# Kernel optimization log

Measured on AMD Instinct MI355X. Metric: run time of the kernel, lower is better.

## Reference

```python
import jax, jax.numpy as jnp
import numpy as np

D = 256; DFFN = 1024; H = 8; NLVL = 4; NPNT = 4; HD = D // H
BS = 4; NQ = 100; NPTS = 25
SPATIAL = [(128, 128), (64, 64), (32, 32), (16, 16)]
LEN_IN = sum(h * w for h, w in SPATIAL)


def _ln(x, g, b, eps=1e-5):
    m = x.mean(-1, keepdims=True)
    v = ((x - m) ** 2).mean(-1, keepdims=True)
    return (x - m) * jax.lax.rsqrt(v + eps) * g + b


def _mha(q, k, v, w_in, b_in, w_out, b_out):
    # torch nn.MultiheadAttention math, batch-first layout [B,S,D]
    B, Sq, _ = q.shape; Sk = k.shape[1]
    wq, wk, wv = jnp.split(w_in, 3, 0); bq, bk, bv = jnp.split(b_in, 3)
    qh = (q @ wq.T + bq).reshape(B, Sq, H, HD).transpose(0, 2, 1, 3)
    kh = (k @ wk.T + bk).reshape(B, Sk, H, HD).transpose(0, 2, 1, 3)
    vh = (v @ wv.T + bv).reshape(B, Sk, H, HD).transpose(0, 2, 1, 3)
    a = jax.nn.softmax(jnp.einsum('bhqd,bhkd->bhqk', qh, kh) * (1.0 / float(np.sqrt(HD))), -1)
    o = jnp.einsum('bhqk,bhkd->bhqd', a, vh).transpose(0, 2, 1, 3).reshape(B, Sq, D)
    return o @ w_out.T + b_out


def _msdeform(query, ref, src, off_w, off_b, aw_w, aw_b, val_w, val_b, out_w, out_b):
    # MSDeformAttn: per-query multi-level bilinear sampling + weighted aggregation
    bs, Lq, _ = query.shape
    value = (src @ val_w.T + val_b).reshape(bs, LEN_IN, H, HD)
    off = (query @ off_w.T + off_b).reshape(bs, Lq, H, NLVL, NPNT, 2)
    aw = jax.nn.softmax((query @ aw_w.T + aw_b).reshape(bs, Lq, H, NLVL * NPNT), -1)
    aw = aw.reshape(bs, Lq, H, NLVL, NPNT)
    norm = jnp.array([[w, h] for h, w in SPATIAL], jnp.float32)  # (W,H) per level
    loc = ref[:, :, None, :, None, :] + off / norm[None, None, None, :, None, :]
    out = jnp.zeros((bs, H, Lq, HD), query.dtype)
    start = 0
    for l, (hh, ww) in enumerate(SPATIAL):
        v_l = value[:, start:start + hh * ww].transpose(0, 2, 1, 3)  # [bs,H,hw,HD]
        start += hh * ww
        # grid_sample align_corners=False pixel coords: loc*size - 0.5
        x = (loc[:, :, :, l, :, 0] * ww - 0.5).transpose(0, 2, 1, 3).reshape(bs, H, Lq * NPNT)
        y = (loc[:, :, :, l, :, 1] * hh - 0.5).transpose(0, 2, 1, 3).reshape(bs, H, Lq * NPNT)
        x0 = jnp.floor(x); y0 = jnp.floor(y); wx = x - x0; wy = y - y0
        x0i = x0.astype(jnp.int32); y0i = y0.astype(jnp.int32); x1i = x0i + 1; y1i = y0i + 1
        def g(xi, yi):
            valid = ((xi >= 0) & (xi < ww) & (yi >= 0) & (yi < hh)).astype(query.dtype)
            idx = jnp.clip(yi, 0, hh - 1) * ww + jnp.clip(xi, 0, ww - 1)
            return jnp.take_along_axis(v_l, idx[..., None], axis=2) * valid[..., None]
        s = (g(x0i, y0i) * ((1 - wx) * (1 - wy))[..., None]
             + g(x1i, y0i) * (wx * (1 - wy))[..., None]
             + g(x0i, y1i) * ((1 - wx) * wy)[..., None]
             + g(x1i, y1i) * (wx * wy)[..., None])
        s = s.reshape(bs, H, Lq, NPNT, HD)
        out = out + (s * aw[:, :, :, l].transpose(0, 2, 1, 3)[..., None]).sum(3)
    return out.transpose(0, 2, 1, 3).reshape(bs, Lq, D) @ out_w.T + out_b


def _fwd(tgt, query_pos, reference_points, src,
         w_in_intra, b_in_intra, w_out_intra, b_out_intra, g_norm_intra, b_norm_intra,
         w_in_inter, b_in_inter, w_out_inter, b_out_inter, g_norm_inter, b_norm_inter,
         off_w, off_b, aw_w, aw_b, val_w, val_b, co_w, co_b, g_norm_cross, b_norm_cross,
         lin1_w, lin1_b, lin2_w, lin2_b, g_norm3, b_norm3):
    bs, nq, npts, d = tgt.shape
    # intra-instance self-attention (over control points)
    q = (tgt + query_pos).reshape(bs * nq, npts, d)
    t2 = _mha(q, q, tgt.reshape(bs * nq, npts, d), w_in_intra, b_in_intra, w_out_intra, b_out_intra)
    tgt = _ln(tgt + t2.reshape(bs, nq, npts, d), g_norm_intra, b_norm_intra)
    # inter-instance self-attention (over queries), no pos embed per source code
    ti = tgt.transpose(0, 2, 1, 3).reshape(bs * npts, nq, d)
    t2 = _mha(ti, ti, ti, w_in_inter, b_in_inter, w_out_inter, b_out_inter)
    ti = _ln(ti + t2, g_norm_inter, b_norm_inter).reshape(bs, npts, nq, d).transpose(0, 2, 1, 3)
    # deformable cross-attention
    ref = jnp.broadcast_to(reference_points[:, :, None], (bs, nq, npts, NLVL, 2)).reshape(bs, nq * npts, NLVL, 2)
    qc = (ti + query_pos).reshape(bs, nq * npts, d)
    t2 = _msdeform(qc, ref, src, off_w, off_b, aw_w, aw_b, val_w, val_b, co_w, co_b).reshape(bs, nq, npts, d)
    tgt = _ln(ti + t2, g_norm_cross, b_norm_cross)
    # FFN
    ff = jax.nn.relu(tgt @ lin1_w.T + lin1_b) @ lin2_w.T + lin2_b
    return _ln(tgt + ff, g_norm3, b_norm3)


def setup_inputs() -> dict:
    key = jax.random.key(0)
    ki = iter(jax.random.split(key, 40))
    def rn(shape, sc=0.02):
        return jax.random.normal(next(ki), shape, jnp.float32) * sc
    inp = dict(
        tgt=jax.random.normal(next(ki), (BS, NQ, NPTS, D), jnp.float32),
        query_pos=jax.random.normal(next(ki), (BS, NQ, NPTS, D), jnp.float32),
        reference_points=jax.random.uniform(next(ki), (BS, NQ, NLVL, 2), jnp.float32),
        src=jax.random.normal(next(ki), (BS, LEN_IN, D), jnp.float32),
        w_in_intra=rn((3 * D, D)), b_in_intra=jnp.zeros((3 * D,), jnp.float32),
        w_out_intra=rn((D, D)), b_out_intra=jnp.zeros((D,), jnp.float32),
        g_norm_intra=jnp.ones((D,), jnp.float32), b_norm_intra=jnp.zeros((D,), jnp.float32),
        w_in_inter=rn((3 * D, D)), b_in_inter=jnp.zeros((3 * D,), jnp.float32),
        w_out_inter=rn((D, D)), b_out_inter=jnp.zeros((D,), jnp.float32),
        g_norm_inter=jnp.ones((D,), jnp.float32), b_norm_inter=jnp.zeros((D,), jnp.float32),
        off_w=rn((H * NLVL * NPNT * 2, D), 0.001), off_b=rn((H * NLVL * NPNT * 2,), 0.5),
        aw_w=rn((H * NLVL * NPNT, D)), aw_b=jnp.zeros((H * NLVL * NPNT,), jnp.float32),
        val_w=rn((D, D)), val_b=jnp.zeros((D,), jnp.float32),
        co_w=rn((D, D)), co_b=jnp.zeros((D,), jnp.float32),
        g_norm_cross=jnp.ones((D,), jnp.float32), b_norm_cross=jnp.zeros((D,), jnp.float32),
        lin1_w=rn((DFFN, D)), lin1_b=jnp.zeros((DFFN,), jnp.float32),
        lin2_w=rn((D, DFFN)), lin2_b=jnp.zeros((D,), jnp.float32),
        g_norm3=jnp.ones((D,), jnp.float32), b_norm3=jnp.zeros((D,), jnp.float32),
        src_spatial_shapes=jnp.array(SPATIAL, jnp.int32),
        level_start_index=jnp.array(np.cumsum([0] + [h * w for h, w in SPATIAL[:-1]]), jnp.int32),
    )
    return inp


def reference(tgt, query_pos, reference_points, src,
              w_in_intra, b_in_intra, w_out_intra, b_out_intra, g_norm_intra, b_norm_intra,
              w_in_inter, b_in_inter, w_out_inter, b_out_inter, g_norm_inter, b_norm_inter,
              off_w, off_b, aw_w, aw_b, val_w, val_b, co_w, co_b, g_norm_cross, b_norm_cross,
              lin1_w, lin1_b, lin2_w, lin2_b, g_norm3, b_norm3,
              src_spatial_shapes, level_start_index):
    # spatial shapes / level starts are compile-time constants (SPATIAL); args kept for signature parity
    return _fwd(tgt, query_pos, reference_points, src,
                w_in_intra, b_in_intra, w_out_intra, b_out_intra, g_norm_intra, b_norm_intra,
                w_in_inter, b_in_inter, w_out_inter, b_out_inter, g_norm_inter, b_norm_inter,
                off_w, off_b, aw_w, aw_b, val_w, val_b, co_w, co_b, g_norm_cross, b_norm_cross,
                lin1_w, lin1_b, lin2_w, lin2_b, g_norm3, b_norm3)
```

## Files before the change

### kernel.cpp

```cpp
#include <hip/hip_runtime.h>
#include <math.h>

#define DMODEL 256
#define HEADS  8
#define HDIM   32
#define BS     4
#define NQ     100
#define NPTS   25
#define LQ     2500
#define M10K   10000
#define LEN_IN 21760
#define MVAL   87040

typedef float f32x4 __attribute__((ext_vector_type(4)));
typedef short s16x8 __attribute__((ext_vector_type(8)));
typedef unsigned short u16;

static __device__ __forceinline__ short f2bf(float f) {
    unsigned u = __builtin_bit_cast(unsigned, f);
    u = (u + 0x7fffu + ((u >> 16) & 1u)) >> 16;
    return (short)u;
}
static __device__ __forceinline__ unsigned pack2(float lo, float hi) {
    return (unsigned)(u16)f2bf(lo) | ((unsigned)(u16)f2bf(hi) << 16);
}
static __device__ __forceinline__ float bf_lo(unsigned u) {
    return __builtin_bit_cast(float, u << 16);
}
static __device__ __forceinline__ float bf_hi(unsigned u) {
    return __builtin_bit_cast(float, u & 0xffff0000u);
}

#define LDSK   40
#define LDSK64 72

__global__ __launch_bounds__(256) void convert_weights_kernel(
    const float* __restrict__ s0, const float* __restrict__ s1,
    const float* __restrict__ s2, const float* __restrict__ s3,
    const float* __restrict__ s4, const float* __restrict__ s5,
    const float* __restrict__ s6, const float* __restrict__ s7,
    const float* __restrict__ s8, const float* __restrict__ s9,
    u16* __restrict__ dst)
{
    int t8 = (blockIdx.x * 256 + threadIdx.x) * 8;
    if (t8 >= 1277952) return;
    const float* s; int base;
    if      (t8 <  196608) { s = s0; base = 0;       }
    else if (t8 <  262144) { s = s1; base = 196608;  }
    else if (t8 <  458752) { s = s2; base = 262144;  }
    else if (t8 <  524288) { s = s3; base = 458752;  }
    else if (t8 <  589824) { s = s4; base = 524288;  }
    else if (t8 <  622592) { s = s5; base = 589824;  }
    else if (t8 <  688128) { s = s6; base = 622592;  }
    else if (t8 <  753664) { s = s7; base = 688128;  }
    else if (t8 < 1015808) { s = s8; base = 753664;  }
    else                   { s = s9; base = 1015808; }
    const float* p = s + (t8 - base);
    float4 a = *(const float4*)p;
    float4 b = *(const float4*)(p + 4);
    s16x8 v;
    v[0]=f2bf(a.x); v[1]=f2bf(a.y); v[2]=f2bf(a.z); v[3]=f2bf(a.w);
    v[4]=f2bf(b.x); v[5]=f2bf(b.y); v[6]=f2bf(b.z); v[7]=f2bf(b.w);
    *(s16x8*)(dst + t8) = v;
}

__global__ __launch_bounds__(256) void add_convert_kernel(
    const float* __restrict__ a, const float* __restrict__ b,
    u16* __restrict__ xb, u16* __restrict__ ab, int n8)
{
    int i = blockIdx.x * 256 + threadIdx.x;
    if (i >= n8) return;
    size_t o = (size_t)i * 8;
    float4 a0 = *(const float4*)(a + o);
    float4 a1 = *(const float4*)(a + o + 4);
    if (ab) {
        s16x8 v;
        v[0]=f2bf(a0.x); v[1]=f2bf(a0.y); v[2]=f2bf(a0.z); v[3]=f2bf(a0.w);
        v[4]=f2bf(a1.x); v[5]=f2bf(a1.y); v[6]=f2bf(a1.z); v[7]=f2bf(a1.w);
        *(s16x8*)(ab + o) = v;
    }
    if (b) {
        float4 b0 = *(const float4*)(b + o);
        float4 b1 = *(const float4*)(b + o + 4);
        a0.x += b0.x; a0.y += b0.y; a0.z += b0.z; a0.w += b0.w;
        a1.x += b1.x; a1.y += b1.y; a1.z += b1.z; a1.w += b1.w;
    }
    s16x8 v;
    v[0]=f2bf(a0.x); v[1]=f2bf(a0.y); v[2]=f2bf(a0.z); v[3]=f2bf(a0.w);
    v[4]=f2bf(a1.x); v[5]=f2bf(a1.y); v[6]=f2bf(a1.z); v[7]=f2bf(a1.w);
    *(s16x8*)(xb + o) = v;
}

__global__ __launch_bounds__(256) void gemm_mfma_kernel(
    const u16* __restrict__ A, int lda,
    const u16* __restrict__ W, int K,
    const float* __restrict__ bias,
    void* __restrict__ Cv, int ldc,
    int M, int relu, int out_bf16)
{
    __shared__ short As[64 * LDSK64];
    __shared__ short Ws[64 * LDSK64];

    const int tid = threadIdx.x;
    const int m0 = blockIdx.y * 64, n0 = blockIdx.x * 64;
    const int srow = tid >> 2;
    const int sk = (tid & 3) * 16;
    const int wave = tid >> 6;
    const int wm = wave & 1, wn = wave >> 1;
    const int lane = tid & 63;
    const int lrow = lane & 15;
    const int kq = lane >> 4;

    const int gm = m0 + srow;
    const u16* aptr = A + (size_t)gm * lda + sk;
    const u16* wptr = W + (size_t)(n0 + srow) * K + sk;

    f32x4 acc[2][2];
#pragma unroll
    for (int i = 0; i < 2; ++i)
#pragma unroll
        for (int j = 0; j < 2; ++j) acc[i][j] = (f32x4)(0.f);

    s16x8 a0 = (s16x8)0, a1 = (s16x8)0, w0, w1;
    if (gm < M) { a0 = *(const s16x8*)aptr; a1 = *(const s16x8*)(aptr + 8); }
    w0 = *(const s16x8*)wptr; w1 = *(const s16x8*)(wptr + 8);

    for (int k0 = 0; k0 < K; k0 += 64) {
        *(s16x8*)&As[srow * LDSK64 + sk]     = a0;
        *(s16x8*)&As[srow * LDSK64 + sk + 8] = a1;
        *(s16x8*)&Ws[srow * LDSK64 + sk]     = w0;
        *(s16x8*)&Ws[srow * LDSK64 + sk + 8] = w1;
        __syncthreads();
        if (k0 + 64 < K) {
            if (gm < M) {
                a0 = *(const s16x8*)(aptr + k0 + 64);
                a1 = *(const s16x8*)(aptr + k0 + 72);
            }
            w0 = *(const s16x8*)(wptr + k0 + 64);
            w1 = *(const s16x8*)(wptr + k0 + 72);
        }

#pragma unroll
        for (int s = 0; s < 2; ++s) {
            s16x8 af[2], bfv[2];
#pragma unroll
            for (int i = 0; i < 2; ++i)
                af[i] = *(const s16x8*)&As[(wm * 32 + i * 16 + lrow) * LDSK64 + s * 32 + kq * 8];
#pragma unroll
            for (int j = 0; j < 2; ++j)
                bfv[j] = *(const s16x8*)&Ws[(wn * 32 + j * 16 + lrow) * LDSK64 + s * 32 + kq * 8];
#pragma unroll
            for (int i = 0; i < 2; ++i)
#pragma unroll
                for (int j = 0; j < 2; ++j)
                    acc[i][j] = __builtin_amdgcn_mfma_f32_16x16x32_bf16(af[i], bfv[j], acc[i][j], 0, 0, 0);
        }
        __syncthreads();
    }

#pragma unroll
    for (int i = 0; i < 2; ++i)
#pragma unroll
        for (int j = 0; j < 2; ++j) {
            int col = n0 + wn * 32 + j * 16 + lrow;
            float bv = bias[col];
#pragma unroll
            for (int reg = 0; reg < 4; ++reg) {
                int gmo = m0 + wm * 32 + i * 16 + kq * 4 + reg;
                if (gmo < M) {
                    float v = acc[i][j][reg] + bv;
                    if (relu) v = fmaxf(v, 0.f);
                    if (out_bf16)
                        ((u16*)Cv)[(size_t)gmo * ldc + col] = (u16)f2bf(v);
                    else
                        ((float*)Cv)[(size_t)gmo * ldc + col] = v;
                }
            }
        }
}

__global__ __launch_bounds__(256) void gemm_mfma128_kernel(
    const u16* __restrict__ A, int lda,
    const u16* __restrict__ W, int K,
    const float* __restrict__ bias,
    void* __restrict__ Cv, int ldc,
    int M, int relu, int out_bf16)
{
    __shared__ short As[128 * LDSK];
    __shared__ short Ws[128 * LDSK];

    const int tid = threadIdx.x;
    const int m0 = blockIdx.y * 128, n0 = blockIdx.x * 128;

    const int srow = tid >> 1;
    const int sk = (tid & 1) * 16;

    const int wave = tid >> 6;
    const int wm = wave & 1, wn = wave >> 1;
    const int lane = tid & 63;
    const int lrow = lane & 15;
    const int kq = lane >> 4;

    const int gm = m0 + srow;
    const u16* aptr = A + (size_t)gm * lda + sk;
    const u16* wptr = W + (size_t)(n0 + srow) * K + sk;

    f32x4 acc[4][4];
#pragma unroll
    for (int i = 0; i < 4; ++i)
#pragma unroll
        for (int j = 0; j < 4; ++j) acc[i][j] = (f32x4)(0.f);

    s16x8 a0 = (s16x8)0, a1 = (s16x8)0, w0, w1;
    if (gm < M) { a0 = *(const s16x8*)aptr; a1 = *(const s16x8*)(aptr + 8); }
    w0 = *(const s16x8*)wptr; w1 = *(const s16x8*)(wptr + 8);

    for (int k0 = 0; k0 < K; k0 += 32) {
        *(s16x8*)&As[srow * LDSK + sk]     = a0;
        *(s16x8*)&As[srow * LDSK + sk + 8] = a1;
        *(s16x8*)&Ws[srow * LDSK + sk]     = w0;
        *(s16x8*)&Ws[srow * LDSK + sk + 8] = w1;
        __syncthreads();
        if (k0 + 32 < K) {
            if (gm < M) {
                a0 = *(const s16x8*)(aptr + k0 + 32);
                a1 = *(const s16x8*)(aptr + k0 + 40);
            }
            w0 = *(const s16x8*)(wptr + k0 + 32);
            w1 = *(const s16x8*)(wptr + k0 + 40);
        }

        s16x8 af[4], bfv[4];
#pragma unroll
        for (int i = 0; i < 4; ++i)
            af[i] = *(const s16x8*)&As[(wm * 64 + i * 16 + lrow) * LDSK + kq * 8];
#pragma unroll
        for (int j = 0; j < 4; ++j)
            bfv[j] = *(const s16x8*)&Ws[(wn * 64 + j * 16 + lrow) * LDSK + kq * 8];
#pragma unroll
        for (int i = 0; i < 4; ++i)
#pragma unroll
            for (int j = 0; j < 4; ++j)
                acc[i][j] = __builtin_amdgcn_mfma_f32_16x16x32_bf16(af[i], bfv[j], acc[i][j], 0, 0, 0);
        __syncthreads();
    }

#pragma unroll
    for (int i = 0; i < 4; ++i)
#pragma unroll
        for (int j = 0; j < 4; ++j) {
            int col = n0 + wn * 64 + j * 16 + lrow;
            float bv = bias[col];
#pragma unroll
            for (int reg = 0; reg < 4; ++reg) {
                int gmo = m0 + wm * 64 + i * 16 + kq * 4 + reg;
                if (gmo < M) {
                    float v = acc[i][j][reg] + bv;
                    if (relu) v = fmaxf(v, 0.f);
                    if (out_bf16)
                        ((u16*)Cv)[(size_t)gmo * ldc + col] = (u16)f2bf(v);
                    else
                        ((float*)Cv)[(size_t)gmo * ldc + col] = v;
                }
            }
        }
}

__global__ __launch_bounds__(256) void gemm_value64_kernel(
    const float* __restrict__ A,
    const u16* __restrict__ W,
    const float* __restrict__ bias,
    u16* __restrict__ C)
{
    __shared__ short As[64 * LDSK];
    __shared__ short Ws[128 * LDSK];

    const int tid = threadIdx.x;
    const int n0 = blockIdx.x * 128;
    const int m0 = blockIdx.y * 64;

    const int arow = tid >> 2;
    const int ak = (tid & 3) * 8;
    const int wrow = tid >> 1;
    const int wk = (tid & 1) * 16;

    const float* aptr = A + (size_t)(m0 + arow) * 256 + ak;
    const u16* wptr = W + (size_t)(n0 + wrow) * 256 + wk;

    const int wave = tid >> 6;
    const int wm = wave & 1, wn = wave >> 1;
    const int lane = tid & 63;
    const int lrow = lane & 15, kq = lane >> 4;

    f32x4 acc[2][4];
#pragma unroll
    for (int i = 0; i < 2; ++i)
#pragma unroll
        for (int j = 0; j < 4; ++j) acc[i][j] = (f32x4)(0.f);

    float4 pa0 = *(const float4*)aptr;
    float4 pa1 = *(const float4*)(aptr + 4);
    s16x8 w0 = *(const s16x8*)wptr;
    s16x8 w1 = *(const s16x8*)(wptr + 8);

    for (int k0 = 0; k0 < 256; k0 += 32) {
        s16x8 av;
        av[0]=f2bf(pa0.x); av[1]=f2bf(pa0.y); av[2]=f2bf(pa0.z); av[3]=f2bf(pa0.w);
        av[4]=f2bf(pa1.x); av[5]=f2bf(pa1.y); av[6]=f2bf(pa1.z); av[7]=f2bf(pa1.w);
        *(s16x8*)&As[arow * LDSK + ak]     = av;
        *(s16x8*)&Ws[wrow * LDSK + wk]     = w0;
        *(s16x8*)&Ws[wrow * LDSK + wk + 8] = w1;
        __syncthreads();
        if (k0 + 32 < 256) {
            pa0 = *(const float4*)(aptr + k0 + 32);
            pa1 = *(const float4*)(aptr + k0 + 36);
            w0 = *(const s16x8*)(wptr + k0 + 32);
            w1 = *(const s16x8*)(wptr + k0 + 40);
        }

        s16x8 af[2], bfv[4];
#pragma unroll
        for (int i = 0; i < 2; ++i)
            af[i] = *(const s16x8*)&As[(wm * 32 + i * 16 + lrow) * LDSK + kq * 8];
#pragma unroll
        for (int j = 0; j < 4; ++j)
            bfv[j] = *(const s16x8*)&Ws[(wn * 64 + j * 16 + lrow) * LDSK + kq * 8];
#pragma unroll
        for (int i = 0; i < 2; ++i)
#pragma unroll
            for (int j = 0; j < 4; ++j)
                acc[i][j] = __builtin_amdgcn_mfma_f32_16x16x32_bf16(af[i], bfv[j], acc[i][j], 0, 0, 0);
        __syncthreads();
    }

#pragma unroll
    for (int i = 0; i < 2; ++i)
#pragma unroll
        for (int j = 0; j < 4; ++j) {
            int col = n0 + wn * 64 + j * 16 + lrow;
            float bv = bias[col];
#pragma unroll
            for (int reg = 0; reg < 4; ++reg) {
                int gmo = m0 + wm * 32 + i * 16 + kq * 4 + reg;
                C[(size_t)gmo * 256 + col] = (u16)f2bf(acc[i][j][reg] + bv);
            }
        }
}

__global__ __launch_bounds__(256) void inter_attn_mfma_kernel(
    const u16* __restrict__ qkv, u16* __restrict__ out, float scale)
{
    __shared__ __align__(16) u16 Qs[112 * 40];
    __shared__ __align__(16) u16 Ks[112 * 40];
    __shared__ __align__(16) u16 Vt[32 * 136];
    __shared__ __align__(16) u16 Ps[112 * 136];

    const int b = blockIdx.x, h = blockIdx.y;
    const u16* base = qkv + (size_t)b * 100 * 768;
    const int tid = threadIdx.x;
    const int wave = tid >> 6, lane = tid & 63;
    const int lr = lane & 15, quad = lane >> 4;

    for (int i = tid; i < 12 * 20; i += 256) {
        int row = 100 + i / 20, c = (i % 20) * 2;
        *(unsigned*)&Qs[row * 40 + c] = 0;
        *(unsigned*)&Ks[row * 40 + c] = 0;
    }
    for (int i = tid; i < 2176; i += 256) ((unsigned*)Vt)[i] = 0;
    for (int i = tid; i < 7616; i += 256) ((unsigned*)Ps)[i] = 0;
    __syncthreads();

    for (int idx = tid; idx < 2400; idx += 256) {
        int row = idx / 24, s = idx % 24;
        const u16* p = (s < 8)  ? base + row * 768 + h * 32 + s * 4
                     : (s < 16) ? base + row * 768 + 256 + h * 32 + (s - 8) * 4
                                : base + row * 768 + 512 + h * 32 + (s - 16) * 4;
        if (s < 8) {
// ... 116 lines not shown
                float4 kf = kr[c4];
                dot = fmaf(q[c4*4+0], kf.x, dot);
                dot = fmaf(q[c4*4+1], kf.y, dot);
                dot = fmaf(q[c4*4+2], kf.z, dot);
                dot = fmaf(q[c4*4+3], kf.w, dot);
            }
            dot *= scale;
            float mn = fmaxf(m, dot);
            float alpha = __expf(m - mn);
            float p = __expf(dot - mn);
            l = l * alpha + p;
            const float4* vr = &KV[j][64 + h * 8];
#pragma unroll
            for (int c4 = 0; c4 < 8; ++c4) {
                float4 vf = vr[c4];
                acc[c4*4+0] = acc[c4*4+0] * alpha + p * vf.x;
                acc[c4*4+1] = acc[c4*4+1] * alpha + p * vf.y;
                acc[c4*4+2] = acc[c4*4+2] * alpha + p * vf.z;
                acc[c4*4+3] = acc[c4*4+3] * alpha + p * vf.w;
            }
            m = mn;
        }
        float inv = 1.f / l;
        unsigned* op = (unsigned*)(out + ((size_t)b * 25 + r) * 256 + h * 32);
#pragma unroll
        for (int c = 0; c < 16; ++c)
            op[c] = pack2(acc[2*c] * inv, acc[2*c+1] * inv);
    }
}

__global__ __launch_bounds__(64) void add_ln_kernel(
    const float* __restrict__ a, const float* __restrict__ b,
    const float* __restrict__ g, const float* __restrict__ beta,
    float* __restrict__ out, u16* __restrict__ out_bf, int transpose_mode)
{
    const int r = blockIdx.x;
    const int lane = threadIdx.x;
    const float* ar = a + (size_t)r * 256;
    const float* br = b + (size_t)r * 256;
    float x[4];
    float s = 0.f;
#pragma unroll
    for (int i = 0; i < 4; ++i) {
        x[i] = ar[lane + 64 * i] + br[lane + 64 * i];
        s += x[i];
    }
#pragma unroll
    for (int off = 32; off >= 1; off >>= 1) s += __shfl_xor(s, off);
    float mean = s * (1.f / 256.f);
    float vs = 0.f;
#pragma unroll
    for (int i = 0; i < 4; ++i) { float d = x[i] - mean; vs += d * d; }
#pragma unroll
    for (int off = 32; off >= 1; off >>= 1) vs += __shfl_xor(vs, off);
    float rstd = rsqrtf(vs * (1.f / 256.f) + 1e-5f);

    size_t ro = r;
    if (transpose_mode == 1) {
        int q = r % 100; int bp = r / 100; int p = bp % 25; int bb = bp / 25;
        ro = ((size_t)bb * 100 + q) * 25 + p;
    } else if (transpose_mode == 2) {
        int p = r % 25; int t = r / 25; int q = t % 100; int bb = t / 100;
        ro = ((size_t)bb * 25 + p) * 100 + q;
    }
    float* orow = out + ro * 256;
    u16* brow = out_bf ? out_bf + ro * 256 : (u16*)0;
#pragma unroll
    for (int i = 0; i < 4; ++i) {
        int c = lane + 64 * i;
        float v = (x[i] - mean) * rstd * g[c] + beta[c];
        orow[c] = v;
        if (brow) brow[c] = (u16)f2bf(v);
    }
}

__global__ __launch_bounds__(256, 4) void msdeform_sample_kernel(
    const u16* __restrict__ value,
    const float* __restrict__ off,
    const float* __restrict__ awl,
    const float* __restrict__ refp,
    u16* __restrict__ sampled)
{
    const int unit = blockIdx.x * 8 + (threadIdx.x >> 5);
    const int t = threadIdx.x & 31;
    const int h = t >> 2, c8 = t & 3;
    const int b = unit / LQ, lq = unit - b * LQ;
    const int q = lq / NPTS;

    const float* awp = awl + (size_t)unit * 128 + h * 16;
    float w[16];
    float mx = -1e30f;
#pragma unroll
    for (int k = 0; k < 16; ++k) { w[k] = awp[k]; mx = fmaxf(mx, w[k]); }
    float sum = 0.f;
#pragma unroll
    for (int k = 0; k < 16; ++k) { w[k] = __expf(w[k] - mx); sum += w[k]; }
    const float inv = 1.f / sum;

    const float* offp = off + (size_t)unit * 256 + h * 32;
    const float* rp = refp + ((size_t)b * 100 + q) * 8;
    const u16* vbase = value + (size_t)b * LEN_IN * 256 + h * 32 + c8 * 8;

    float acc[8];
#pragma unroll
    for (int k = 0; k < 8; ++k) acc[k] = 0.f;
// ... 85 lines not shown
    const float* co_b       = (const float*)d_in[23];
    const float* g_ln_cross = (const float*)d_in[24];
    const float* b_ln_cross = (const float*)d_in[25];
    const float* lin1_w     = (const float*)d_in[26];
    const float* lin1_b     = (const float*)d_in[27];
    const float* lin2_w     = (const float*)d_in[28];
    const float* lin2_b     = (const float*)d_in[29];
    const float* g_ln3      = (const float*)d_in[30];
    const float* b_ln3      = (const float*)d_in[31];

    float* ws    = (float*)d_ws;
    float* qkv   = ws;
    float* tmp   = ws + 7680000;
    u16*   attnb = (u16*)(ws + 10240000);
    float* tgt1  = ws + 11520000;
    float* ti    = ws + 14080000;
    u16*   tib   = (u16*)(ws + 16640000);
    float* tA    = ws + 17920000;
    u16*   qcb   = (u16*)(ws + 20480000);
    u16*   x1b   = (u16*)(ws + 21760000);
    u16*   tgtb  = (u16*)(ws + 23040000);
    float* awl   = ws + 24320000;
    u16*   valueb= (u16*)(ws + 25600000);
    u16*   wb    = (u16*)(ws + 36741120);
    float* out   = (float*)d_out;

    u16* qkvb = (u16*)qkv;

    u16* wb_in_intra  = wb;
    u16* wb_out_intra = wb + 196608;
    u16* wb_in_inter  = wb + 262144;
    u16* wb_out_inter = wb + 458752;
    u16* wb_off       = wb + 524288;
    u16* wb_aw        = wb + 589824;
    u16* wb_val       = wb + 622592;
    u16* wb_co        = wb + 688128;
    u16* wb_lin1      = wb + 753664;
    u16* wb_lin2      = wb + 1015808;

    const float scale = 0.17677669529663687f;
    const int MB64  = (M10K + 63) / 64;
    const int MB128 = (M10K + 127) / 128;

    convert_weights_kernel<<<624, 256, 0, stream>>>(
        w_in_intra, w_out_intra, w_in_inter, w_out_inter, off_w,
        aw_w, val_w, co_w, lin1_w, lin2_w, wb);
    add_convert_kernel<<<1250, 256, 0, stream>>>(tgt, query_pos, x1b, tgtb, 320000);

    gemm_mfma128_kernel<<<dim3(4, MB128), 256, 0, stream>>>(x1b, 256, wb_in_intra, 256,
                                                            b_in_intra, qkv, 768, M10K, 0, 0);
    gemm_mfma_kernel<<<dim3(4, MB64), 256, 0, stream>>>(tgtb, 256, wb_in_intra + 512 * 256, 256,
                                                        b_in_intra + 512, qkv + 512, 768, M10K, 0, 0);
    intra_attn_kernel<<<400, 256, 0, stream>>>(qkv, attnb, scale);
    gemm_mfma_kernel<<<dim3(4, MB64), 256, 0, stream>>>(attnb, 256, wb_out_intra, 256,
                                                        b_out_intra, tmp, 256, M10K, 0, 0);
    add_ln_kernel<<<M10K, 64, 0, stream>>>(tgt, tmp, g_ln_intra, b_ln_intra, ti, tib, 2);

    gemm_mfma128_kernel<<<dim3(6, MB128), 256, 0, stream>>>(tib, 256, wb_in_inter, 256,
                                                            b_in_inter, qkvb, 768, M10K, 0, 1);
    inter_attn_mfma_kernel<<<dim3(100, 8), 256, 0, stream>>>(qkvb, attnb, scale);
    gemm_mfma_kernel<<<dim3(4, MB64), 256, 0, stream>>>(attnb, 256, wb_out_inter, 256,
                                                        b_out_inter, tmp, 256, M10K, 0, 0);
    add_ln_kernel<<<M10K, 64, 0, stream>>>(ti, tmp, g_ln_inter, b_ln_inter, tA, (u16*)0, 1);

    add_convert_kernel<<<1250, 256, 0, stream>>>(tA, query_pos, qcb, (u16*)0, 320000);
    gemm_value64_kernel<<<dim3(2, 1360), 256, 0, stream>>>(src, wb_val, val_b, valueb);
    gemm_mfma_kernel<<<dim3(4, MB64), 256, 0, stream>>>(qcb, 256, wb_off, 256,
                                                        off_b, tgt1, 256, M10K, 0, 0);
    gemm_mfma_kernel<<<dim3(2, MB64), 256, 0, stream>>>(qcb, 256, wb_aw, 256,
                                                        aw_b, awl, 128, M10K, 0, 0);
    msdeform_sample_kernel<<<1250, 256, 0, stream>>>(valueb, tgt1, awl, refp, attnb);
    gemm_mfma_kernel<<<dim3(4, MB64), 256, 0, stream>>>(attnb, 256, wb_co, 256,
                                                        co_b, tmp, 256, M10K, 0, 0);
    add_ln_kernel<<<M10K, 64, 0, stream>>>(tA, tmp, g_ln_cross, b_ln_cross, ti, tib, 0);

    gemm_mfma128_kernel<<<dim3(8, MB128), 256, 0, stream>>>(tib, 256, wb_lin1, 256,
                                                            lin1_b, valueb, 1024, M10K, 1, 1);
    gemm_mfma_kernel<<<dim3(4, MB64), 256, 0, stream>>>(valueb, 1024, wb_lin2, 1024,
                                                        lin2_b, tmp, 256, M10K, 0, 0);
    add_ln_kernel<<<M10K, 64, 0, stream>>>(ti, tmp, g_ln3, b_ln3, out, (u16*)0, 0);
}
```

Before: 479.2 us.

## Merge independent launches into fat kernels and fuse query_pos add into LayerNorm

Weight conversion and the tgt/query_pos conversion now run as one launch, selected by block index. The value projection and the intra-attention QKV GEMMs are merged into one multi-role launch, so the large value GEMM overlaps with the QKV work. The offset and attention-weight GEMMs share one launch through a column split, and the query_pos add plus bf16 conversion moves into the inter LayerNorm epilogue, removing one elementwise kernel. This cuts launch count and idle tails, at the cost of mixed-role blocks with different shared-memory and register needs, which may lower occupancy.

```diff
diff --git a/kernel.cpp b/kernel.cpp
--- a/kernel.cpp
+++ b/kernel.cpp
@@ -34,250 +34,68 @@
 #define LDSK   40
 #define LDSK64 72
 
-__global__ __launch_bounds__(256) void convert_weights_kernel(
+__global__ __launch_bounds__(256) void fat_stage0_kernel(
     const float* __restrict__ s0, const float* __restrict__ s1,
     const float* __restrict__ s2, const float* __restrict__ s3,
     const float* __restrict__ s4, const float* __restrict__ s5,
     const float* __restrict__ s6, const float* __restrict__ s7,
     const float* __restrict__ s8, const float* __restrict__ s9,
-    u16* __restrict__ dst)
-{
-    int t8 = (blockIdx.x * 256 + threadIdx.x) * 8;
-    if (t8 >= 1277952) return;
-    const float* s; int base;
-    if      (t8 <  196608) { s = s0; base = 0;       }
-    else if (t8 <  262144) { s = s1; base = 196608;  }
-    else if (t8 <  458752) { s = s2; base = 262144;  }
-    else if (t8 <  524288) { s = s3; base = 458752;  }
-    else if (t8 <  589824) { s = s4; base = 524288;  }
-    else if (t8 <  622592) { s = s5; base = 589824;  }
-    else if (t8 <  688128) { s = s6; base = 622592;  }
-    else if (t8 <  753664) { s = s7; base = 688128;  }
-    else if (t8 < 1015808) { s = s8; base = 753664;  }
-    else                   { s = s9; base = 1015808; }
-    const float* p = s + (t8 - base);
-    float4 a = *(const float4*)p;
-    float4 b = *(const float4*)(p + 4);
-    s16x8 v;
-    v[0]=f2bf(a.x); v[1]=f2bf(a.y); v[2]=f2bf(a.z); v[3]=f2bf(a.w);
-    v[4]=f2bf(b.x); v[5]=f2bf(b.y); v[6]=f2bf(b.z); v[7]=f2bf(b.w);
-    *(s16x8*)(dst + t8) = v;
-}
-
-__global__ __launch_bounds__(256) void add_convert_kernel(
+    u16* __restrict__ dst,
     const float* __restrict__ a, const float* __restrict__ b,
-    u16* __restrict__ xb, u16* __restrict__ ab, int n8)
-{
-    int i = blockIdx.x * 256 + threadIdx.x;
-    if (i >= n8) return;
-    size_t o = (size_t)i * 8;
-    float4 a0 = *(const float4*)(a + o);
-    float4 a1 = *(const float4*)(a + o + 4);
-    if (ab) {
+    u16* __restrict__ xb, u16* __restrict__ ab)
+{
+    if (blockIdx.x < 624) {
+        int t8 = (blockIdx.x * 256 + threadIdx.x) * 8;
+        if (t8 >= 1277952) return;
+        const float* s; int base;
+        if      (t8 <  196608) { s = s0; base = 0;       }
+        else if (t8 <  262144) { s = s1; base = 196608;  }
+        else if (t8 <  458752) { s = s2; base = 262144;  }
+        else if (t8 <  524288) { s = s3; base = 458752;  }
+        else if (t8 <  589824) { s = s4; base = 524288;  }
+        else if (t8 <  622592) { s = s5; base = 589824;  }
+        else if (t8 <  688128) { s = s6; base = 622592;  }
+        else if (t8 <  753664) { s = s7; base = 688128;  }
+        else if (t8 < 1015808) { s = s8; base = 753664;  }
+        else                   { s = s9; base = 1015808; }
+        const float* p = s + (t8 - base);
+        float4 fa = *(const float4*)p;
+        float4 fb = *(const float4*)(p + 4);
+        s16x8 v;
+        v[0]=f2bf(fa.x); v[1]=f2bf(fa.y); v[2]=f2bf(fa.z); v[3]=f2bf(fa.w);
+        v[4]=f2bf(fb.x); v[5]=f2bf(fb.y); v[6]=f2bf(fb.z); v[7]=f2bf(fb.w);
+        *(s16x8*)(dst + t8) = v;
+    } else {
+        int i = (blockIdx.x - 624) * 256 + threadIdx.x;
+        size_t o = (size_t)i * 8;
+        float4 a0 = *(const float4*)(a + o);
+        float4 a1 = *(const float4*)(a + o + 4);
         s16x8 v;
         v[0]=f2bf(a0.x); v[1]=f2bf(a0.y); v[2]=f2bf(a0.z); v[3]=f2bf(a0.w);
         v[4]=f2bf(a1.x); v[5]=f2bf(a1.y); v[6]=f2bf(a1.z); v[7]=f2bf(a1.w);
         *(s16x8*)(ab + o) = v;
-    }
-    if (b) {
         float4 b0 = *(const float4*)(b + o);
         float4 b1 = *(const float4*)(b + o + 4);
         a0.x += b0.x; a0.y += b0.y; a0.z += b0.z; a0.w += b0.w;
         a1.x += b1.x; a1.y += b1.y; a1.z += b1.z; a1.w += b1.w;
-    }
-    s16x8 v;
-    v[0]=f2bf(a0.x); v[1]=f2bf(a0.y); v[2]=f2bf(a0.z); v[3]=f2bf(a0.w);
-    v[4]=f2bf(a1.x); v[5]=f2bf(a1.y); v[6]=f2bf(a1.z); v[7]=f2bf(a1.w);
-    *(s16x8*)(xb + o) = v;
-}
-
-__global__ __launch_bounds__(256) void gemm_mfma_kernel(
-    const u16* __restrict__ A, int lda,
-    const u16* __restrict__ W, int K,
-    const float* __restrict__ bias,
-    void* __restrict__ Cv, int ldc,
-    int M, int relu, int out_bf16)
-{
-    __shared__ short As[64 * LDSK64];
-    __shared__ short Ws[64 * LDSK64];
+        s16x8 w;
+        w[0]=f2bf(a0.x); w[1]=f2bf(a0.y); w[2]=f2bf(a0.z); w[3]=f2bf(a0.w);
+        w[4]=f2bf(a1.x); w[5]=f2bf(a1.y); w[6]=f2bf(a1.z); w[7]=f2bf(a1.w);
+        *(s16x8*)(xb + o) = w;
+    }
+}
+
+
+static __device__ __forceinline__ void body_value64(
+    char* smem_, const float* __restrict__ A, const u16* __restrict__ W,
+    const float* __restrict__ bias, u16* __restrict__ C, int bx, int by)
+{
+    short* As = (short*)smem_;
+    short* Ws = (short*)(smem_ + 5120);
 
     const int tid = threadIdx.x;
-    const int m0 = blockIdx.y * 64, n0 = blockIdx.x * 64;
-    const int srow = tid >> 2;
-    const int sk = (tid & 3) * 16;
-    const int wave = tid >> 6;
-    const int wm = wave & 1, wn = wave >> 1;
-    const int lane = tid & 63;
-    const int lrow = lane & 15;
-    const int kq = lane >> 4;
-
-    const int gm = m0 + srow;
-    const u16* aptr = A + (size_t)gm * lda + sk;
-    const u16* wptr = W + (size_t)(n0 + srow) * K + sk;
-
-    f32x4 acc[2][2];
-#pragma unroll
-    for (int i = 0; i < 2; ++i)
-#pragma unroll
-        for (int j = 0; j < 2; ++j) acc[i][j] = (f32x4)(0.f);
-
-    s16x8 a0 = (s16x8)0, a1 = (s16x8)0, w0, w1;
-    if (gm < M) { a0 = *(const s16x8*)aptr; a1 = *(const s16x8*)(aptr + 8); }
-    w0 = *(const s16x8*)wptr; w1 = *(const s16x8*)(wptr + 8);
-
-    for (int k0 = 0; k0 < K; k0 += 64) {
-        *(s16x8*)&As[srow * LDSK64 + sk]     = a0;
-        *(s16x8*)&As[srow * LDSK64 + sk + 8] = a1;
-        *(s16x8*)&Ws[srow * LDSK64 + sk]     = w0;
-        *(s16x8*)&Ws[srow * LDSK64 + sk + 8] = w1;
-        __syncthreads();
-        if (k0 + 64 < K) {
-            if (gm < M) {
-                a0 = *(const s16x8*)(aptr + k0 + 64);
-                a1 = *(const s16x8*)(aptr + k0 + 72);
-            }
-            w0 = *(const s16x8*)(wptr + k0 + 64);
-            w1 = *(const s16x8*)(wptr + k0 + 72);
-        }
-
-#pragma unroll
-        for (int s = 0; s < 2; ++s) {
-            s16x8 af[2], bfv[2];
-#pragma unroll
-            for (int i = 0; i < 2; ++i)
-                af[i] = *(const s16x8*)&As[(wm * 32 + i * 16 + lrow) * LDSK64 + s * 32 + kq * 8];
-#pragma unroll
-            for (int j = 0; j < 2; ++j)
-                bfv[j] = *(const s16x8*)&Ws[(wn * 32 + j * 16 + lrow) * LDSK64 + s * 32 + kq * 8];
-#pragma unroll
-            for (int i = 0; i < 2; ++i)
-#pragma unroll
-                for (int j = 0; j < 2; ++j)
-                    acc[i][j] = __builtin_amdgcn_mfma_f32_16x16x32_bf16(af[i], bfv[j], acc[i][j], 0, 0, 0);
-        }
-        __syncthreads();
-    }
-
-#pragma unroll
-    for (int i = 0; i < 2; ++i)
-#pragma unroll
-        for (int j = 0; j < 2; ++j) {
-            int col = n0 + wn * 32 + j * 16 + lrow;
-            float bv = bias[col];
-#pragma unroll
-            for (int reg = 0; reg < 4; ++reg) {
-                int gmo = m0 + wm * 32 + i * 16 + kq * 4 + reg;
-                if (gmo < M) {
-                    float v = acc[i][j][reg] + bv;
-                    if (relu) v = fmaxf(v, 0.f);
-                    if (out_bf16)
-                        ((u16*)Cv)[(size_t)gmo * ldc + col] = (u16)f2bf(v);
-                    else
-                        ((float*)Cv)[(size_t)gmo * ldc + col] = v;
-                }
-            }
-        }
-}
-
-__global__ __launch_bounds__(256) void gemm_mfma128_kernel(
-    const u16* __restrict__ A, int lda,
-    const u16* __restrict__ W, int K,
-    const float* __restrict__ bias,
-    void* __restrict__ Cv, int ldc,
-    int M, int relu, int out_bf16)
-{
-    __shared__ short As[128 * LDSK];
-    __shared__ short Ws[128 * LDSK];
-
-    const int tid = threadIdx.x;
-    const int m0 = blockIdx.y * 128, n0 = blockIdx.x * 128;
-
-    const int srow = tid >> 1;
-    const int sk = (tid & 1) * 16;
-
-    const int wave = tid >> 6;
-    const int wm = wave & 1, wn = wave >> 1;
-    const int lane = tid & 63;
-    const int lrow = lane & 15;
-    const int kq = lane >> 4;
-
-    const int gm = m0 + srow;
-    const u16* aptr = A + (size_t)gm * lda + sk;
-    const u16* wptr = W + (size_t)(n0 + srow) * K + sk;
-
-    f32x4 acc[4][4];
-#pragma unroll
-    for (int i = 0; i < 4; ++i)
-#pragma unroll
-        for (int j = 0; j < 4; ++j) acc[i][j] = (f32x4)(0.f);
-
-    s16x8 a0 = (s16x8)0, a1 = (s16x8)0, w0, w1;
-    if (gm < M) { a0 = *(const s16x8*)aptr; a1 = *(const s16x8*)(aptr + 8); }
-    w0 = *(const s16x8*)wptr; w1 = *(const s16x8*)(wptr + 8);
-
-    for (int k0 = 0; k0 < K; k0 += 32) {
-        *(s16x8*)&As[srow * LDSK + sk]     = a0;
-        *(s16x8*)&As[srow * LDSK + sk + 8] = a1;
-        *(s16x8*)&Ws[srow * LDSK + sk]     = w0;
-        *(s16x8*)&Ws[srow * LDSK + sk + 8] = w1;
-        __syncthreads();
-        if (k0 + 32 < K) {
-            if (gm < M) {
-                a0 = *(const s16x8*)(aptr + k0 + 32);
-                a1 = *(const s16x8*)(aptr + k0 + 40);
-            }
-            w0 = *(const s16x8*)(wptr + k0 + 32);
-            w1 = *(const s16x8*)(wptr + k0 + 40);
-        }
-
-        s16x8 af[4], bfv[4];
-#pragma unroll
-        for (int i = 0; i < 4; ++i)
-            af[i] = *(const s16x8*)&As[(wm * 64 + i * 16 + lrow) * LDSK + kq * 8];
-#pragma unroll
-        for (int j = 0; j < 4; ++j)
-            bfv[j] = *(const s16x8*)&Ws[(wn * 64 + j * 16 + lrow) * LDSK + kq * 8];
-#pragma unroll
-        for (int i = 0; i < 4; ++i)
-#pragma unroll
-            for (int j = 0; j < 4; ++j)
-                acc[i][j] = __builtin_amdgcn_mfma_f32_16x16x32_bf16(af[i], bfv[j], acc[i][j], 0, 0, 0);
-        __syncthreads();
-    }
-
-#pragma unroll
-    for (int i = 0; i < 4; ++i)
-#pragma unroll
-        for (int j = 0; j < 4; ++j) {
-            int col = n0 + wn * 64 + j * 16 + lrow;
-            float bv = bias[col];
-#pragma unroll
-            for (int reg = 0; reg < 4; ++reg) {
-                int gmo = m0 + wm * 64 + i * 16 + kq * 4 + reg;
-                if (gmo < M) {
-                    float v = acc[i][j][reg] + bv;
-                    if (relu) v = fmaxf(v, 0.f);
-                    if (out_bf16)
-                        ((u16*)Cv)[(size_t)gmo * ldc + col] = (u16)f2bf(v);
-                    else
-                        ((float*)Cv)[(size_t)gmo * ldc + col] = v;
-                }
-            }
-        }
-}
-
-__global__ __launch_bounds__(256) void gemm_value64_kernel(
-    const float* __restrict__ A,
-    const u16* __restrict__ W,
-    const float* __restrict__ bias,
-    u16* __restrict__ C)
-{
-    __shared__ short As[64 * LDSK];
-    __shared__ short Ws[128 * LDSK];
-
-    const int tid = threadIdx.x;
-    const int n0 = blockIdx.x * 128;
-    const int m0 = blockIdx.y * 64;
+    const int n0 = bx * 128;
+    const int m0 = by * 64;
 
     const int arow = tid >> 2;
     const int ak = (tid & 3) * 8;
@@ -343,6 +161,361 @@
             for (int reg = 0; reg < 4; ++reg) {
                 int gmo = m0 + wm * 32 + i * 16 + kq * 4 + reg;
                 C[(size_t)gmo * 256 + col] = (u16)f2bf(acc[i][j][reg] + bv);
+            }
+        }
+}
+
+static __device__ __forceinline__ void body_mfma128(
+    char* smem_, const u16* __restrict__ A, const u16* __restrict__ W,
+    const float* __restrict__ bias, float* __restrict__ Cv, int bx, int by)
+{
+    short* As = (short*)smem_;
+    short* Ws = (short*)(smem_ + 10240);
+
+    const int tid = threadIdx.x;
+    const int m0 = by * 128, n0 = bx * 128;
+    const int srow = tid >> 1;
+    const int sk = (tid & 1) * 16;
+    const int wave = tid >> 6;
+    const int wm = wave & 1, wn = wave >> 1;
+    const int lane = tid & 63;
+    const int lrow = lane & 15, kq = lane >> 4;
+
+    const int gm = m0 + srow;
+    const u16* aptr = A + (size_t)gm * 256 + sk;
+    const u16* wptr = W + (size_t)(n0 + srow) * 256 + sk;
+
+    f32x4 acc[4][4];
+#pragma unroll
+    for (int i = 0; i < 4; ++i)
+#pragma unroll
+        for (int j = 0; j < 4; ++j) acc[i][j] = (f32x4)(0.f);
+
+    s16x8 a0 = (s16x8)0, a1 = (s16x8)0, w0, w1;
+    if (gm < M10K) { a0 = *(const s16x8*)aptr; a1 = *(const s16x8*)(aptr + 8); }
+    w0 = *(const s16x8*)wptr; w1 = *(const s16x8*)(wptr + 8);
+
+    for (int k0 = 0; k0 < 256; k0 += 32) {
+        *(s16x8*)&As[srow * LDSK + sk]     = a0;
+        *(s16x8*)&As[srow * LDSK + sk + 8] = a1;
+        *(s16x8*)&Ws[srow * LDSK + sk]     = w0;
+        *(s16x8*)&Ws[srow * LDSK + sk + 8] = w1;
+        __syncthreads();
+        if (k0 + 32 < 256) {
+            if (gm < M10K) {
+                a0 = *(const s16x8*)(aptr + k0 + 32);
+                a1 = *(const s16x8*)(aptr + k0 + 40);
+            }
+            w0 = *(const s16x8*)(wptr + k0 + 32);
+            w1 = *(const s16x8*)(wptr + k0 + 40);
+        }
+
+        s16x8 af[4], bfv[4];
+#pragma unroll
+        for (int i = 0; i < 4; ++i)
+            af[i] = *(const s16x8*)&As[(wm * 64 + i * 16 + lrow) * LDSK + kq * 8];
+#pragma unroll
+        for (int j = 0; j < 4; ++j)
+            bfv[j] = *(const s16x8*)&Ws[(wn * 64 + j * 16 + lrow) * LDSK + kq * 8];
+#pragma unroll
+        for (int i = 0; i < 4; ++i)
+#pragma unroll
+            for (int j = 0; j < 4; ++j)
+                acc[i][j] = __builtin_amdgcn_mfma_f32_16x16x32_bf16(af[i], bfv[j], acc[i][j], 0, 0, 0);
+        __syncthreads();
+    }
+
+#pragma unroll
+    for (int i = 0; i < 4; ++i)
+#pragma unroll
+        for (int j = 0; j < 4; ++j) {
+            int col = n0 + wn * 64 + j * 16 + lrow;
+            float bv = bias[col];
+#pragma unroll
+            for (int reg = 0; reg < 4; ++reg) {
+                int gmo = m0 + wm * 64 + i * 16 + kq * 4 + reg;
+                if (gmo < M10K)
+                    Cv[(size_t)gmo * 768 + col] = acc[i][j][reg] + bv;
+            }
+        }
+}
+
+static __device__ __forceinline__ void body_mfma64(
+    char* smem_, const u16* __restrict__ A, const u16* __restrict__ W,
+    const float* __restrict__ bias, float* __restrict__ Cv, int bx, int by)
+{
+    short* As = (short*)smem_;
+    short* Ws = (short*)(smem_ + 9216);
+
+    const int tid = threadIdx.x;
+    const int m0 = by * 64, n0 = bx * 64;
+    const int srow = tid >> 2;
+    const int sk = (tid & 3) * 16;
+    const int wave = tid >> 6;
+    const int wm = wave & 1, wn = wave >> 1;
+    const int lane = tid & 63;
+    const int lrow = lane & 15, kq = lane >> 4;
+
+    const int gm = m0 + srow;
+    const u16* aptr = A + (size_t)gm * 256 + sk;
+    const u16* wptr = W + (size_t)(n0 + srow) * 256 + sk;
+
+    f32x4 acc[2][2];
+#pragma unroll
+    for (int i = 0; i < 2; ++i)
+#pragma unroll
+        for (int j = 0; j < 2; ++j) acc[i][j] = (f32x4)(0.f);
+
+    s16x8 a0 = (s16x8)0, a1 = (s16x8)0, w0, w1;
+    if (gm < M10K) { a0 = *(const s16x8*)aptr; a1 = *(const s16x8*)(aptr + 8); }
+    w0 = *(const s16x8*)wptr; w1 = *(const s16x8*)(wptr + 8);
+
+    for (int k0 = 0; k0 < 256; k0 += 64) {
+        *(s16x8*)&As[srow * LDSK64 + sk]     = a0;
+        *(s16x8*)&As[srow * LDSK64 + sk + 8] = a1;
+        *(s16x8*)&Ws[srow * LDSK64 + sk]     = w0;
+        *(s16x8*)&Ws[srow * LDSK64 + sk + 8] = w1;
+        __syncthreads();
+        if (k0 + 64 < 256) {
+            if (gm < M10K) {
+                a0 = *(const s16x8*)(aptr + k0 + 64);
+                a1 = *(const s16x8*)(aptr + k0 + 72);
+            }
+            w0 = *(const s16x8*)(wptr + k0 + 64);
+            w1 = *(const s16x8*)(wptr + k0 + 72);
+        }
+
+#pragma unroll
+        for (int s = 0; s < 2; ++s) {
+            s16x8 af[2], bfv[2];
+#pragma unroll
+            for (int i = 0; i < 2; ++i)
+                af[i] = *(const s16x8*)&As[(wm * 32 + i * 16 + lrow) * LDSK64 + s * 32 + kq * 8];
+#pragma unroll
+            for (int j = 0; j < 2; ++j)
+                bfv[j] = *(const s16x8*)&Ws[(wn * 32 + j * 16 + lrow) * LDSK64 + s * 32 + kq * 8];
+#pragma unroll
+            for (int i = 0; i < 2; ++i)
+#pragma unroll
+                for (int j = 0; j < 2; ++j)
+                    acc[i][j] = __builtin_amdgcn_mfma_f32_16x16x32_bf16(af[i], bfv[j], acc[i][j], 0, 0, 0);
+        }
+        __syncthreads();
+    }
+
+#pragma unroll
+    for (int i = 0; i < 2; ++i)
+#pragma unroll
+        for (int j = 0; j < 2; ++j) {
+            int col = n0 + wn * 32 + j * 16 + lrow;
+            float bv = bias[col];
+#pragma unroll
+            for (int reg = 0; reg < 4; ++reg) {
+                int gmo = m0 + wm * 32 + i * 16 + kq * 4 + reg;
+                if (gmo < M10K)
+                    Cv[(size_t)gmo * 768 + col] = acc[i][j][reg] + bv;
+            }
+        }
+}
+
+__global__ __launch_bounds__(256) void fat_stage1_kernel(
+    const float* __restrict__ src, const u16* __restrict__ wval,
+    const float* __restrict__ valb, u16* __restrict__ valueb,
+    const u16* __restrict__ x1b, const u16* __restrict__ wqk,
+    const float* __restrict__ bqk, float* __restrict__ qkv,
+    const u16* __restrict__ tgtb, const u16* __restrict__ wv,
+    const float* __restrict__ bv, float* __restrict__ qkv_v)
+{
+    __shared__ __align__(16) char smem[20480];
+    const int b = blockIdx.x;
+    if (b < 2720) {
+        body_value64(smem, src, wval, valb, valueb, b & 1, b >> 1);
+    } else if (b < 3036) {
+        const int bb = b - 2720;
+        body_mfma128(smem, x1b, wqk, bqk, qkv, bb & 3, bb >> 2);
+    } else {
+        const int bb = b - 3036;
+        body_mfma64(smem, tgtb, wv, bv, qkv_v, bb & 3, bb >> 2);
+    }
+}
+
+__global__ __launch_bounds__(256) void gemm_mfma_kernel(
+    const u16* __restrict__ A, int lda,
+    const u16* __restrict__ W, int K,
+    const float* __restrict__ bias,
+    void* __restrict__ Cv, int ldc,
+    int M, int relu, int out_bf16,
+    int ncut, const float* __restrict__ bias2,
+    float* __restrict__ Cv2, int ldc2)
+{
+    __shared__ short As[64 * LDSK64];
+    __shared__ short Ws[64 * LDSK64];
+
+    const int tid = threadIdx.x;
+    const int m0 = blockIdx.y * 64, n0 = blockIdx.x * 64;
+    const int srow = tid >> 2;
+    const int sk = (tid & 3) * 16;
+    const int wave = tid >> 6;
+    const int wm = wave & 1, wn = wave >> 1;
+    const int lane = tid & 63;
+    const int lrow = lane & 15;
+    const int kq = lane >> 4;
+
+    const int gm = m0 + srow;
+    const u16* aptr = A + (size_t)gm * lda + sk;
+    const u16* wptr = W + (size_t)(n0 + srow) * K + sk;
+
+    f32x4 acc[2][2];
+#pragma unroll
+    for (int i = 0; i < 2; ++i)
+#pragma unroll
+        for (int j = 0; j < 2; ++j) acc[i][j] = (f32x4)(0.f);
+
+    s16x8 a0 = (s16x8)0, a1 = (s16x8)0, w0, w1;
+    if (gm < M) { a0 = *(const s16x8*)aptr; a1 = *(const s16x8*)(aptr + 8); }
+    w0 = *(const s16x8*)wptr; w1 = *(const s16x8*)(wptr + 8);
+
+    for (int k0 = 0; k0 < K; k0 += 64) {
+        *(s16x8*)&As[srow * LDSK64 + sk]     = a0;
+        *(s16x8*)&As[srow * LDSK64 + sk + 8] = a1;
+        *(s16x8*)&Ws[srow * LDSK64 + sk]     = w0;
+        *(s16x8*)&Ws[srow * LDSK64 + sk + 8] = w1;
+        __syncthreads();
+        if (k0 + 64 < K) {
+            if (gm < M) {
+                a0 = *(const s16x8*)(aptr + k0 + 64);
+                a1 = *(const s16x8*)(aptr + k0 + 72);
+            }
+            w0 = *(const s16x8*)(wptr + k0 + 64);
+            w1 = *(const s16x8*)(wptr + k0 + 72);
+        }
+
+#pragma unroll
+        for (int s = 0; s < 2; ++s) {
+            s16x8 af[2], bfv[2];
+#pragma unroll
+            for (int i = 0; i < 2; ++i)
+                af[i] = *(const s16x8*)&As[(wm * 32 + i * 16 + lrow) * LDSK64 + s * 32 + kq * 8];
+#pragma unroll
+            for (int j = 0; j < 2; ++j)
+                bfv[j] = *(const s16x8*)&Ws[(wn * 32 + j * 16 + lrow) * LDSK64 + s * 32 + kq * 8];
+#pragma unroll
+            for (int i = 0; i < 2; ++i)
+#pragma unroll
+                for (int j = 0; j < 2; ++j)
+                    acc[i][j] = __builtin_amdgcn_mfma_f32_16x16x32_bf16(af[i], bfv[j], acc[i][j], 0, 0, 0);
+        }
+        __syncthreads();
+    }
+
+#pragma unroll
+    for (int i = 0; i < 2; ++i)
+#pragma unroll
+        for (int j = 0; j < 2; ++j) {
+            int col = n0 + wn * 32 + j * 16 + lrow;
+            float bv = (col < ncut) ? bias[col] : bias2[col - ncut];
+#pragma unroll
+            for (int reg = 0; reg < 4; ++reg) {
+                int gmo = m0 + wm * 32 + i * 16 + kq * 4 + reg;
+                if (gmo < M) {
+                    float v = acc[i][j][reg] + bv;
+                    if (relu) v = fmaxf(v, 0.f);
+                    if (col < ncut) {
+                        if (out_bf16)
+                            ((u16*)Cv)[(size_t)gmo * ldc + col] = (u16)f2bf(v);
+                        else
+                            ((float*)Cv)[(size_t)gmo * ldc + col] = v;
+                    } else {
+                        Cv2[(size_t)gmo * ldc2 + (col - ncut)] = v;
+                    }
+                }
+            }
+        }
+}
+
+__global__ __launch_bounds__(256) void gemm_mfma128_kernel(
+    const u16* __restrict__ A, int lda,
+    const u16* __restrict__ W, int K,
+    const float* __restrict__ bias,
+    void* __restrict__ Cv, int ldc,
+    int M, int relu, int out_bf16)
+{
+    __shared__ short As[128 * LDSK];
+    __shared__ short Ws[128 * LDSK];
+
+    const int tid = threadIdx.x;
+    const int m0 = blockIdx.y * 128, n0 = blockIdx.x * 128;
+
+    const int srow = tid >> 1;
+    const int sk = (tid & 1) * 16;
+
+    const int wave = tid >> 6;
+    const int wm = wave & 1, wn = wave >> 1;
+    const int lane = tid & 63;
+    const int lrow = lane & 15;
+    const int kq = lane >> 4;
+
+    const int gm = m0 + srow;
+    const u16* aptr = A + (size_t)gm * lda + sk;
+    const u16* wptr = W + (size_t)(n0 + srow) * K + sk;
+
+    f32x4 acc[4][4];
+#pragma unroll
+    for (int i = 0; i < 4; ++i)
+#pragma unroll
+        for (int j = 0; j < 4; ++j) acc[i][j] = (f32x4)(0.f);
+
+    s16x8 a0 = (s16x8)0, a1 = (s16x8)0, w0, w1;
+    if (gm < M) { a0 = *(const s16x8*)aptr; a1 = *(const s16x8*)(aptr + 8); }
+    w0 = *(const s16x8*)wptr; w1 = *(const s16x8*)(wptr + 8);
+
+    for (int k0 = 0; k0 < K; k0 += 32) {
+        *(s16x8*)&As[srow * LDSK + sk]     = a0;
+        *(s16x8*)&As[srow * LDSK + sk + 8] = a1;
+        *(s16x8*)&Ws[srow * LDSK + sk]     = w0;
+        *(s16x8*)&Ws[srow * LDSK + sk + 8] = w1;
+        __syncthreads();
+        if (k0 + 32 < K) {
+            if (gm < M) {
+                a0 = *(const s16x8*)(aptr + k0 + 32);
+                a1 = *(const s16x8*)(aptr + k0 + 40);
+            }
+            w0 = *(const s16x8*)(wptr + k0 + 32);
+            w1 = *(const s16x8*)(wptr + k0 + 40);
+        }
+
+        s16x8 af[4], bfv[4];
+#pragma unroll
+        for (int i = 0; i < 4; ++i)
+            af[i] = *(const s16x8*)&As[(wm * 64 + i * 16 + lrow) * LDSK + kq * 8];
+#pragma unroll
+        for (int j = 0; j < 4; ++j)
+            bfv[j] = *(const s16x8*)&Ws[(wn * 64 + j * 16 + lrow) * LDSK + kq * 8];
+#pragma unroll
+        for (int i = 0; i < 4; ++i)
+#pragma unroll
+            for (int j = 0; j < 4; ++j)
+                acc[i][j] = __builtin_amdgcn_mfma_f32_16x16x32_bf16(af[i], bfv[j], acc[i][j], 0, 0, 0);
+        __syncthreads();
+    }
+
+#pragma unroll
+    for (int i = 0; i < 4; ++i)
+#pragma unroll
+        for (int j = 0; j < 4; ++j) {
+            int col = n0 + wn * 64 + j * 16 + lrow;
+            float bv = bias[col];
+#pragma unroll
+            for (int reg = 0; reg < 4; ++reg) {
+                int gmo = m0 + wm * 64 + i * 16 + kq * 4 + reg;
+                if (gmo < M) {
+                    float v = acc[i][j][reg] + bv;
+                    if (relu) v = fmaxf(v, 0.f);
+                    if (out_bf16)
+                        ((u16*)Cv)[(size_t)gmo * ldc + col] = (u16)f2bf(v);
+                    else
+                        ((float*)Cv)[(size_t)gmo * ldc + col] = v;
+                }
             }
         }
 }
@@ -525,7 +698,9 @@
 __global__ __launch_bounds__(64) void add_ln_kernel(
     const float* __restrict__ a, const float* __restrict__ b,
     const float* __restrict__ g, const float* __restrict__ beta,
-    float* __restrict__ out, u16* __restrict__ out_bf, int transpose_mode)
+    float* __restrict__ out, u16* __restrict__ out_bf,
+    const float* __restrict__ qp, u16* __restrict__ qout,
+    int transpose_mode)
 {
     const int r = blockIdx.x;
     const int lane = threadIdx.x;
@@ -558,12 +733,15 @@
     }
     float* orow = out + ro * 256;
     u16* brow = out_bf ? out_bf + ro * 256 : (u16*)0;
+    const float* qrow = qp ? qp + ro * 256 : (const float*)0;
+    u16* qrow_o = qout ? qout + ro * 256 : (u16*)0;
 #pragma unroll
     for (int i = 0; i < 4; ++i) {
         int c = lane + 64 * i;
         float v = (x[i] - mean) * rstd * g[c] + beta[c];
         orow[c] = v;
         if (brow) brow[c] = (u16)f2bf(v);
+        if (qrow_o) qrow_o[c] = (u16)f2bf(v + qrow[c]);
     }
 }
 
@@ -715,7 +893,6 @@
     u16* wb_in_inter  = wb + 262144;
     u16* wb_out_inter = wb + 458752;
     u16* wb_off       = wb + 524288;
-    u16* wb_aw        = wb + 589824;
     u16* wb_val       = wb + 622592;
     u16* wb_co        = wb + 688128;
     u16* wb_lin1      = wb + 753664;
@@ -724,42 +901,49 @@
     const float scale = 0.17677669529663687f;
     const int MB64  = (M10K + 63) / 64;
     const int MB128 = (M10K + 127) / 128;
-
-    convert_weights_kernel<<<624, 256, 0, stream>>>(
+    const int NC_OFF = 1 << 30;
+
+    fat_stage0_kernel<<<1874, 256, 0, stream>>>(
         w_in_intra, w_out_intra, w_in_inter, w_out_inter, off_w,
-        aw_w, val_w, co_w, lin1_w, lin2_w, wb);
-    add_convert_kernel<<<1250, 256, 0, stream>>>(tgt, query_pos, x1b, tgtb, 320000);
-
-    gemm_mfma128_kernel<<<dim3(4, MB128), 256, 0, stream>>>(x1b, 256, wb_in_intra, 256,
-                                                            b_in_intra, qkv, 768, M10K, 0, 0);
-    gemm_mfma_kernel<<<dim3(4, MB64), 256, 0, stream>>>(tgtb, 256, wb_in_intra + 512 * 256, 256,
-                                                        b_in_intra + 512, qkv + 512, 768, M10K, 0, 0);
+        aw_w, val_w, co_w, lin1_w, lin2_w, wb,
+        tgt, query_pos, x1b, tgtb);
+
+    fat_stage1_kernel<<<3664, 256, 0, stream>>>(
+        src, wb_val, val_b, valueb,
+        x1b, wb_in_intra, b_in_intra, qkv,
+        tgtb, wb_in_intra + 512 * 256, b_in_intra + 512, qkv + 512);
+
     intra_attn_kernel<<<400, 256, 0, stream>>>(qkv, attnb, scale);
     gemm_mfma_kernel<<<dim3(4, MB64), 256, 0, stream>>>(attnb, 256, wb_out_intra, 256,
-                                                        b_out_intra, tmp, 256, M10K, 0, 0);
-    add_ln_kernel<<<M10K, 64, 0, stream>>>(tgt, tmp, g_ln_intra, b_ln_intra, ti, tib, 2);
+                                                        b_out_intra, tmp, 256, M10K, 0, 0,
+                                                        NC_OFF, b_out_intra, (float*)0, 0);
+    add_ln_kernel<<<M10K, 64, 0, stream>>>(tgt, tmp, g_ln_intra, b_ln_intra,
+                                           ti, tib, (const float*)0, (u16*)0, 2);
 
     gemm_mfma128_kernel<<<dim3(6, MB128), 256, 0, stream>>>(tib, 256, wb_in_inter, 256,
                                                             b_in_inter, qkvb, 768, M10K, 0, 1);
     inter_attn_mfma_kernel<<<dim3(100, 8), 256, 0, stream>>>(qkvb, attnb, scale);
     gemm_mfma_kernel<<<dim3(4, MB64), 256, 0, stream>>>(attnb, 256, wb_out_inter, 256,
-                                                        b_out_inter, tmp, 256, M10K, 0, 0);
-    add_ln_kernel<<<M10K, 64, 0, stream>>>(ti, tmp, g_ln_inter, b_ln_inter, tA, (u16*)0, 1);
-
-    add_convert_kernel<<<1250, 256, 0, stream>>>(tA, query_pos, qcb, (u16*)0, 320000);
-    gemm_value64_kernel<<<dim3(2, 1360), 256, 0, stream>>>(src, wb_val, val_b, valueb);
-    gemm_mfma_kernel<<<dim3(4, MB64), 256, 0, stream>>>(qcb, 256, wb_off, 256,
-                                                        off_b, tgt1, 256, M10K, 0, 0);
-    gemm_mfma_kernel<<<dim3(2, MB64), 256, 0, stream>>>(qcb, 256, wb_aw, 256,
-                                                        aw_b, awl, 128, M10K, 0, 0);
+                                                        b_out_inter, tmp, 256, M10K, 0, 0,
+                                                        NC_OFF, b_out_inter, (float*)0, 0);
+    add_ln_kernel<<<M10K, 64, 0, stream>>>(ti, tmp, g_ln_inter, b_ln_inter,
+                                           tA, (u16*)0, query_pos, qcb, 1);
+
+    gemm_mfma_kernel<<<dim3(6, MB64), 256, 0, stream>>>(qcb, 256, wb_off, 256,
+                                                        off_b, tgt1, 256, M10K, 0, 0,
+                                                        256, aw_b, awl, 128);
     msdeform_sample_kernel<<<1250, 256, 0, stream>>>(valueb, tgt1, awl, refp, attnb);
     gemm_mfma_kernel<<<dim3(4, MB64), 256, 0, stream>>>(attnb, 256, wb_co, 256,
-                                                        co_b, tmp, 256, M10K, 0, 0);
-    add_ln_kernel<<<M10K, 64, 0, stream>>>(tA, tmp, g_ln_cross, b_ln_cross, ti, tib, 0);
+                                                        co_b, tmp, 256, M10K, 0, 0,
+                                                        NC_OFF, co_b, (float*)0, 0);
+    add_ln_kernel<<<M10K, 64, 0, stream>>>(tA, tmp, g_ln_cross, b_ln_cross,
+                                           ti, tib, (const float*)0, (u16*)0, 0);
 
     gemm_mfma128_kernel<<<dim3(8, MB128), 256, 0, stream>>>(tib, 256, wb_lin1, 256,
                                                             lin1_b, valueb, 1024, M10K, 1, 1);
     gemm_mfma_kernel<<<dim3(4, MB64), 256, 0, stream>>>(valueb, 1024, wb_lin2, 1024,
-                                                        lin2_b, tmp, 256, M10K, 0, 0);
-    add_ln_kernel<<<M10K, 64, 0, stream>>>(ti, tmp, g_ln3, b_ln3, out, (u16*)0, 0);
-}
+                                                        lin2_b, tmp, 256, M10K, 0, 0,
+                                                        NC_OFF, lin2_b, (float*)0, 0);
+    add_ln_kernel<<<M10K, 64, 0, stream>>>(ti, tmp, g_ln3, b_ln3,
+                                           out, (u16*)0, (const float*)0, (u16*)0, 0);
+}
```

Measured after the change: 458.1 us. 1.05x faster.
